# Kernel optimization log

Hardware: AMD Instinct MI355X
Metric: run time of the kernel (lower is better)

## Reference

```python
import jax, jax.numpy as jnp
import numpy as np

B, N, C = 128, 320, 768
H = 12
T = 64    # template tokens (8x8)
S = 256   # search tokens (16x16)


def setup_inputs() -> dict:
    key = jax.random.key(0)
    k1, k2, k3, k4 = jax.random.split(key, 4)
    return {
        "x1": jax.random.normal(k1, (B, N, C), dtype=jnp.float32),
        "x2": jax.random.normal(k2, (B, N, C), dtype=jnp.float32),
        "qkv_w": jax.random.normal(k3, (3 * C, C), dtype=jnp.float32) * 0.02,
        "proj_w": jax.random.normal(k4, (C, C), dtype=jnp.float32) * 0.02,
        "proj_b": jnp.zeros((C,), dtype=jnp.float32),
    }


def reference(x1, x2, qkv_w, proj_w, proj_b):
    # concat template tokens from x1 with search tokens from x2
    x = jnp.concatenate([x1[:, :T, :], x2[:, T:, :]], axis=1)  # [B, N, C]
    b, n, c = x.shape
    d = c // H
    scale = d ** -0.5

    qkv = (x @ qkv_w.T).reshape(b, n, 3, H, d).transpose(2, 0, 3, 1, 4)  # [3,B,H,N,D]
    q, k, v = qkv[0], qkv[1], qkv[2]

    # template -> template self-attention
    q_mt, k_mt, v_mt = q[:, :, :T], k[:, :, :T], v[:, :, :T]
    attn_mt = jax.nn.softmax(jnp.einsum('bhtd,bhsd->bhts', q_mt, k_mt) * scale, axis=-1)
    x_mt = jnp.einsum('bhts,bhsd->bhtd', attn_mt, v_mt).transpose(0, 2, 1, 3).reshape(b, T, c)

    # search -> all cross+self attention
    q_s = q[:, :, T:]
    attn_s = jax.nn.softmax(jnp.einsum('bhqd,bhkd->bhqk', q_s, k) * scale, axis=-1)
    x_s = jnp.einsum('bhqk,bhkd->bhqd', attn_s, v).transpose(0, 2, 1, 3).reshape(b, S, c)

    out = jnp.concatenate([x_mt, x_s], axis=1) @ proj_w.T + proj_b
    return out
```

## Files before the change

kernel.cpp:

```cpp
#include <hip/hip_runtime.h>
#include <hip/hip_bf16.h>
#include <stdint.h>

#define B_   128
#define N_   320
#define C_   768
#define H_   12
#define D_   64
#define NT_  (B_*N_)
#define K3_  (3*C_)
#define NKT  12
#define TE   (256*64)

typedef __attribute__((ext_vector_type(8))) __bf16 bf16x8;
typedef __attribute__((ext_vector_type(4))) float  f32x4;

__device__ __forceinline__ unsigned short f2bf(float f) {
  union { float f; unsigned u; } v; v.f = f;
  return (unsigned short)((v.u + 0x7fffu + ((v.u >> 16) & 1u)) >> 16);
}

__device__ __forceinline__ void gload16(const unsigned short* g, unsigned short* l) {
  __builtin_amdgcn_global_load_lds((const __attribute__((address_space(1))) void*)g,
                                   (__attribute__((address_space(3))) void*)l,
                                   16, 0, 0);
}

__global__ void prep_x(const float* __restrict__ x1, const float* __restrict__ x2,
                       unsigned short* __restrict__ xb) {
  const unsigned total4 = (unsigned)NT_ * C_ / 4;
  const unsigned stride = gridDim.x * blockDim.x;
  for (unsigned i = blockIdx.x * blockDim.x + threadIdx.x; i < total4; i += stride) {
    unsigned tok = i / (C_ / 4);
    unsigned n   = tok % N_;
    const float* src = (n < 64u) ? x1 : x2;
    float4 v = *(const float4*)(src + (size_t)i * 4u);
    ushort4 o;
    o.x = f2bf(v.x); o.y = f2bf(v.y); o.z = f2bf(v.z); o.w = f2bf(v.w);
    *(ushort4*)(xb + (size_t)i * 4u) = o;
  }
}

__global__ void prep_w(const float* __restrict__ qkv_w, const float* __restrict__ proj_w,
                       unsigned short* __restrict__ wq, unsigned short* __restrict__ wp) {
  const int QKV4 = (K3_ * C_) / 4;
  const int Q4   = (C_ * C_) / 4;
  const int P4   = (C_ * C_) / 4;
  int i = blockIdx.x * 256 + threadIdx.x;
  if (i < QKV4) {
    float s = (i < Q4) ? 0.125f : 1.0f;
    float4 v = *(const float4*)(qkv_w + (size_t)i * 4);
    ushort4 o;
    o.x = f2bf(v.x * s); o.y = f2bf(v.y * s); o.z = f2bf(v.z * s); o.w = f2bf(v.w * s);
    *(ushort4*)(wq + (size_t)i * 4) = o;
  } else if (i < QKV4 + P4) {
    int j = i - QKV4;
    float4 v = *(const float4*)(proj_w + (size_t)j * 4);
    ushort4 o;
    o.x = f2bf(v.x); o.y = f2bf(v.y); o.z = f2bf(v.z); o.w = f2bf(v.w);
    *(ushort4*)(wp + (size_t)j * 4) = o;
  }
}

#define BARR do { asm volatile("" ::: "memory"); __builtin_amdgcn_s_barrier(); asm volatile("" ::: "memory"); } while(0)
#define VMW(n) asm volatile("s_waitcnt vmcnt(" #n ")" ::: "memory")
#define PRIO1 __builtin_amdgcn_s_setprio(1)
#define PRIO0 __builtin_amdgcn_s_setprio(0)
#define RD(base, off) (*(const bf16x8*)((base) + (off)))

#define LDA_Q(ARR, QQ, PARX) do { \
    ARR[0][0] = RD(bAk0, (PARX)*32768 + (QQ)*8192);        \
    ARR[0][1] = RD(bAk1, (PARX)*32768 + (QQ)*8192);        \
    ARR[1][0] = RD(bAk0, (PARX)*32768 + (QQ)*8192 + 2048); \
    ARR[1][1] = RD(bAk1, (PARX)*32768 + (QQ)*8192 + 2048); } while(0)

#define LDB(PARX) do { \
    _Pragma("unroll") for (int nf = 0; nf < 4; ++nf) { \
      b_[0][nf] = RD(bBk0, (PARX)*32768 + nf*2048); \
      b_[1][nf] = RD(bBk1, (PARX)*32768 + nf*2048); } } while(0)

#define MFN(ARR, QQ) do { \
    _Pragma("unroll") for (int ks = 0; ks < 2; ++ks) \
    _Pragma("unroll") for (int f = 0; f < 2; ++f) \
    _Pragma("unroll") for (int nf = 0; nf < 4; ++nf) \
      acc[(QQ)*2+f][nf] = __builtin_amdgcn_mfma_f32_16x16x32_bf16(ARR[f][ks], b_[ks][nf], acc[(QQ)*2+f][nf], 0, 0, 0); \
  } while(0)

#define MFS(ARR, QQ) do { \
    _Pragma("unroll") for (int ks = 0; ks < 2; ++ks) \
    _Pragma("unroll") for (int f = 0; f < 2; ++f) \
    _Pragma("unroll") for (int nf = 0; nf < 4; ++nf) \
      acc[(QQ)*2+f][nf] = __builtin_amdgcn_mfma_f32_16x16x32_bf16(b_[ks][nf], ARR[f][ks], acc[(QQ)*2+f][nf], 0, 0, 0); \
  } while(0)

#define STGA4(PARX) do { \
    gload16(gA00, dA + ((PARX)^1)*TE);        gload16(gA01, dA + ((PARX)^1)*TE + 512);  \
    gload16(gA10, dA + ((PARX)^1)*TE + 8192); gload16(gA11, dA + ((PARX)^1)*TE + 8704); \
    gA00 += 64; gA01 += 64; gA10 += 64; gA11 += 64; } while(0)
#define STGB4(PARX) do { \
    gload16(gB00, dB + ((PARX)^1)*TE);        gload16(gB01, dB + ((PARX)^1)*TE + 512);  \
    gload16(gB10, dB + ((PARX)^1)*TE + 8192); gload16(gB11, dB + ((PARX)^1)*TE + 8704); \
    gB00 += 64; gB01 += 64; gB10 += 64; gB11 += 64; } while(0)
#define STG8(PARX) do { STGA4(PARX); STGB4(PARX); } while(0)

#define KT1(MF, PARX, STG_) do { \
    LDB(PARX); LDA_Q(aL_, 0, PARX); \
    STG_; \
    LDA_Q(aH_, 1, PARX); \
    PRIO1; MF(aL_, 0); PRIO0; \
    LDA_Q(aL_, 2, PARX); \
    PRIO1; MF(aH_, 1); PRIO0; \
    LDA_Q(aH_, 3, PARX); \
    PRIO1; MF(aL_, 2); PRIO0; \
    PRIO1; MF(aH_, 3); PRIO0; \
    VMW(0); BARR; \
  } while(0)

#define RESETA do { \
    gA00 = Ag_ + (size_t)row0n*768 + offA00; gA01 = Ag_ + (size_t)row0n*768 + offA01; \
    gA10 = Ag_ + (size_t)row0n*768 + offA10; gA11 = Ag_ + (size_t)row0n*768 + offA11; } while(0)
#define RESETB do { \
    gB00 = Wg_ + (size_t)col0n*768 + offA00; gB01 = Wg_ + (size_t)col0n*768 + offA01; \
    gB10 = Wg_ + (size_t)col0n*768 + offA10; gB11 = Wg_ + (size_t)col0n*768 + offA11; } while(0)

#define TILE12(MF) do { \
    _Pragma("unroll 1") for (int tt = 0; tt < 5; ++tt) { \
      KT1(MF, 0, STG8(0)); \
      KT1(MF, 1, STG8(1)); \
    } \
    KT1(MF, 0, STG8(0)); \
    KT1(MF, 1, { RESETA; RESETB; STG8(1); }); \
  } while(0)

#define GEMM_SETUP \
  const int tid = threadIdx.x, lane = tid & 63, w = tid >> 6; \
  const int wr = w >> 2, wc = w & 3; \
  const int lr = lane & 15, kg = lane >> 4; \
  const int rr = lane >> 3; \
  const int sp = (lane & 7) ^ rr; \
  const char* bAk0 = (const char*)As + wr*4096 + lr*128 + ((0*4 + kg) ^ (lr & 7))*16; \
  const char* bAk1 = (const char*)As + wr*4096 + lr*128 + ((1*4 + kg) ^ (lr & 7))*16; \
  const char* bBk0 = (const char*)Bs + wc*8192 + lr*128 + ((0*4 + kg) ^ (lr & 7))*16; \
  const char* bBk1 = (const char*)Bs + wc*8192 + lr*128 + ((1*4 + kg) ^ (lr & 7))*16; \
  const size_t offA00 = (size_t)(w*16 + rr)*768 + sp*8; \
  const size_t offA01 = offA00 + (size_t)8*768; \
  const size_t offA10 = offA00 + (size_t)128*768; \
  const size_t offA11 = offA01 + (size_t)128*768; \
  unsigned short* dA = As + w*1024; \
  unsigned short* dB = Bs + w*1024; \
  const unsigned short *gA00, *gA01, *gA10, *gA11, *gB00, *gB01, *gB10, *gB11;

#define GEMM_PROLOGUE(row0i, col0i) do { \
    gA00 = Ag_ + (size_t)(row0i)*768 + offA00; gA01 = Ag_ + (size_t)(row0i)*768 + offA01; \
    gA10 = Ag_ + (size_t)(row0i)*768 + offA10; gA11 = Ag_ + (size_t)(row0i)*768 + offA11; \
    gB00 = Wg_ + (size_t)(col0i)*768 + offA00; gB01 = Wg_ + (size_t)(col0i)*768 + offA01; \
    gB10 = Wg_ + (size_t)(col0i)*768 + offA10; gB11 = Wg_ + (size_t)(col0i)*768 + offA11; \
    STG8(1); \
    VMW(0); BARR; \
  } while(0)

#define ACC_ZERO do { \
    _Pragma("unroll") for (int mf = 0; mf < 8; ++mf) \
    _Pragma("unroll") for (int nf = 0; nf < 4; ++nf) acc[mf][nf] = vzero; } while(0)

__global__ void __launch_bounds__(512) gemm_qkv(const unsigned short* __restrict__ A,
                                                const unsigned short* __restrict__ W,
                                                unsigned short* __restrict__ qb,
                                                unsigned short* __restrict__ kb,
                                                unsigned short* __restrict__ vb) {
  __shared__ __align__(16) unsigned short As[2 * TE];
  __shared__ __align__(16) unsigned short Bs[2 * TE];
  GEMM_SETUP
  const unsigned short* Ag_ = A;
  const unsigned short* Wg_ = W;
  const int wv = blockIdx.x / 80;
  const int lb = blockIdx.x - wv * 80;

  const f32x4 vzero = {0.f, 0.f, 0.f, 0.f};
  f32x4 acc[8][4];
  ACC_ZERO;
  bf16x8 aL_[2][2], aH_[2][2], b_[2][4];

  {
    const int t0i = lb * 6;
    const int row0i = (t0i / 3) * 256, col0i = (wv * 3 + t0i % 3) * 256;
    GEMM_PROLOGUE(row0i, col0i);
  }

  if (wv != 2) {
    unsigned short* dst = (wv == 0) ? qb : kb;
#pragma unroll 1
    for (int j = 0; j < 6; ++j) {
      const int t = lb * 6 + j, tn = (j < 5) ? t + 1 : t;
      const int row0c = (t / 3) * 256, cb = (t % 3) * 256;
      const int row0n = (tn / 3) * 256, col0n = (wv * 3 + tn % 3) * 256;
      TILE12(MFS);
#pragma unroll
      for (int mf = 0; mf < 8; ++mf) {
        const int tok = row0c + (mf >> 1) * 64 + wr * 32 + (mf & 1) * 16 + lr;
        const unsigned bq = (unsigned)tok / 320u;
        const int tt2 = tok - (int)bq * 320;
#pragma unroll
        for (int nf = 0; nf < 4; ++nf) {
          const int nn = cb + wc * 64 + nf * 16 + kg * 4;
          const int h = nn >> 6, dd = nn & 63;
          ushort4 o;
          o.x = f2bf(acc[mf][nf][0]); o.y = f2bf(acc[mf][nf][1]);
          o.z = f2bf(acc[mf][nf][2]); o.w = f2bf(acc[mf][nf][3]);
          *(ushort4*)&dst[(size_t)((((int)bq * 12 + h) * 320 + tt2) * 64 + dd)] = o;
        }
      }
      ACC_ZERO;
    }
  } else {
#pragma unroll 1
    for (int j = 0; j < 6; ++j) {
      const int t = lb * 6 + j, tn = (j < 5) ? t + 1 : t;
      const int row0c = (t / 3) * 256, cb = (t % 3) * 256;
      const int row0n = (tn / 3) * 256, col0n = (wv * 3 + tn % 3) * 256;
      TILE12(MFN);
#pragma unroll
      for (int mf = 0; mf < 8; ++mf) {
        const int m0 = row0c + (mf >> 1) * 64 + wr * 32 + (mf & 1) * 16 + kg * 4;
        const unsigned bq = (unsigned)m0 / 320u;
        const int t0v = m0 - (int)bq * 320;
#pragma unroll
        for (int nf = 0; nf < 4; ++nf) {
          const int nn = cb + wc * 64 + nf * 16 + lr;
          const int h = nn >> 6, dd = nn & 63;
          ushort4 o;
          o.x = f2bf(acc[mf][nf][0]); o.y = f2bf(acc[mf][nf][1]);
          o.z = f2bf(acc[mf][nf][2]); o.w = f2bf(acc[mf][nf][3]);
          *(ushort4*)&vb[(size_t)(((((int)bq * 12 + h) * 64 + dd) * 320) + t0v)] = o;
        }
      }
      ACC_ZERO;
    }
  }
  asm volatile("s_waitcnt vmcnt(0) lgkmcnt(0)" ::: "memory");
}

__global__ void __launch_bounds__(256) attn(const unsigned short* __restrict__ qb,
                                            const unsigned short* __restrict__ kb,
                                            const unsigned short* __restrict__ vb,
                                            unsigned short* __restrict__ ab) {
  __shared__ __align__(16) unsigned short Ks[64 * 64];
  __shared__ __align__(16) unsigned short Vt[64 * 64];
  __shared__ __align__(16) unsigned short Pl[4 * 16 * 64];
  const int bid = blockIdx.x;
  const int qt = bid % 5, bh = bid / 5;
  const int tid = threadIdx.x, lane = tid & 63, w = tid >> 6;
  const int lr = lane & 15, kg = lane >> 4;

  const int qrow = qt * 64 + w * 16 + lr;
  const unsigned short* qptr = qb + (bh * 320 + qrow) * 64;
  const bf16x8 qa0 = *(const bf16x8*)(qptr + kg * 8);
  const bf16x8 qa1 = *(const bf16x8*)(qptr + 32 + kg * 8);

  f32x4 o[4] = {};
  float mrun[4] = {-1e30f, -1e30f, -1e30f, -1e30f};
  float lrun[4] = {0.f, 0.f, 0.f, 0.f};
  const int nchunk = (qt == 0) ? 1 : 5;

  const int c0 = w, c1 = w + 4;
  const int srow0 = c0 * 8 + (lane >> 3);
  const int srow1 = c1 * 8 + (lane >> 3);
  const int slot  = lane & 7;
  const int part0 = slot ^ (srow0 & 7);
  const int part1 = slot ^ (srow1 & 7);
  const unsigned short* kbase = kb + bh * 320 * 64;
  const unsigned short* vbase = vb + bh * 64 * 320;
  unsigned short* lk0 = &Ks[c0 * 512];
  unsigned short* lk1 = &Ks[c1 * 512];
  unsigned short* lv0 = &Vt[c0 * 512];
  unsigned short* lv1 = &Vt[c1 * 512];
  char* PwB = (char*)&Pl[w * 1024];

  for (int kc = 0; kc < nchunk; kc++) {
    gload16(kbase + (kc * 64 + srow0) * 64 + part0 * 8, lk0);
    gload16(kbase + (kc * 64 + srow1) * 64 + part1 * 8, lk1);
    gload16(vbase + srow0 * 320 + kc * 64 + part0 * 8, lv0);
    gload16(vbase + srow1 * 320 + kc * 64 + part1 * 8, lv1);
    __syncthreads();

    f32x4 s[4];
#pragma unroll
    for (int kt = 0; kt < 4; kt++) {
      const int key = kt * 16 + lr;
      const char* kr = (const char*)Ks + key * 128;
      const unsigned sw = (unsigned)((key & 7) << 4);
      bf16x8 k0 = *(const bf16x8*)(kr + ((kg * 16) ^ sw));
      bf16x8 k1 = *(const bf16x8*)(kr + ((64 + kg * 16) ^ sw));
      f32x4 z = {0.f, 0.f, 0.f, 0.f};
      z = __builtin_amdgcn_mfma_f32_16x16x32_bf16(qa0, k0, z, 0, 0, 0);
      z = __builtin_amdgcn_mfma_f32_16x16x32_bf16(qa1, k1, z, 0, 0, 0);
      s[kt] = z;
    }

#pragma unroll
    for (int r = 0; r < 4; r++) {
      float rm = fmaxf(fmaxf(s[0][r], s[1][r]), fmaxf(s[2][r], s[3][r]));
      rm = fmaxf(rm, __shfl_xor(rm, 1));
      rm = fmaxf(rm, __shfl_xor(rm, 2));
      rm = fmaxf(rm, __shfl_xor(rm, 4));
      rm = fmaxf(rm, __shfl_xor(rm, 8));
      const float mn = fmaxf(mrun[r], rm);
      const float alpha = __expf(mrun[r] - mn);
      mrun[r] = mn;
      const int q = kg * 4 + r;
      char* prow = PwB + q * 128;
      const unsigned sw = (unsigned)((q & 7) << 4);
      float rs = 0.f;
#pragma unroll
      for (int kt = 0; kt < 4; kt++) {
        const float p = __expf(s[kt][r] - mn);
        rs += p;
        const int key = kt * 16 + lr;
        *(unsigned short*)(prow + ((key * 2) ^ sw)) = f2bf(p);
      }
      rs += __shfl_xor(rs, 1);
      rs += __shfl_xor(rs, 2);
      rs += __shfl_xor(rs, 4);
      rs += __shfl_xor(rs, 8);
      lrun[r] = lrun[r] * alpha + rs;
#pragma unroll
      for (int dt = 0; dt < 4; dt++) o[dt][r] *= alpha;
    }

    asm volatile("s_waitcnt lgkmcnt(0)" ::: "memory");

    {
      const char* par = (const char*)PwB + lr * 128;
      const unsigned swp = (unsigned)((lr & 7) << 4);
      bf16x8 p0 = *(const bf16x8*)(par + ((kg * 16) ^ swp));
      bf16x8 p1 = *(const bf16x8*)(par + ((64 + kg * 16) ^ swp));
#pragma unroll
      for (int dt = 0; dt < 4; dt++) {
        const int d = dt * 16 + lr;
        const char* vr = (const char*)Vt + d * 128;
        const unsigned swv = (unsigned)((d & 7) << 4);
        bf16x8 v0 = *(const bf16x8*)(vr + ((kg * 16) ^ swv));
        bf16x8 v1 = *(const bf16x8*)(vr + ((64 + kg * 16) ^ swv));
        o[dt] = __builtin_amdgcn_mfma_f32_16x16x32_bf16(p0, v0, o[dt], 0, 0, 0);
        o[dt] = __builtin_amdgcn_mfma_f32_16x16x32_bf16(p1, v1, o[dt], 0, 0, 0);
      }
    }
    __syncthreads();
  }

  const int b = bh / 12, h = bh - b * 12;
#pragma unroll
  for (int r = 0; r < 4; r++) {
    const float inv = 1.0f / lrun[r];
    const int token = b * 320 + qt * 64 + w * 16 + kg * 4 + r;
    unsigned short* orow = ab + token * 768 + h * 64;
#pragma unroll
    for (int dt = 0; dt < 4; dt++)
      orow[dt * 16 + lr] = f2bf(o[dt][r] * inv);
  }
}

__global__ void __launch_bounds__(512) gemm_proj(const unsigned short* __restrict__ A,
                                                 const unsigned short* __restrict__ W,
                                                 const float* __restrict__ bias,
                                                 float* __restrict__ out) {
  __shared__ __align__(16) unsigned short As[2 * TE];
  __shared__ __align__(16) unsigned short Bs[2 * TE];
  GEMM_SETUP
  const unsigned short* Ag_ = A;
  const unsigned short* Wg_ = W;
  const int lb = blockIdx.x;

  const f32x4 vzero = {0.f, 0.f, 0.f, 0.f};
  f32x4 acc[8][4];
  ACC_ZERO;
  bf16x8 aL_[2][2], aH_[2][2], b_[2][4];

  {
    const int t0i = lb * 2;
    const int row0i = (t0i / 3) * 256, col0i = (t0i % 3) * 256;
    GEMM_PROLOGUE(row0i, col0i);
  }

#pragma unroll 1
  for (int j = 0; j < 2; ++j) {
    const int t = lb * 2 + j, tn = (j < 1) ? t + 1 : t;
    const int row0c = (t / 3) * 256, col0c = (t % 3) * 256;
    const int row0n = (tn / 3) * 256, col0n = (tn % 3) * 256;
    TILE12(MFN);
#pragma unroll
    for (int nf = 0; nf < 4; ++nf) {
      const int nn = col0c + wc * 64 + nf * 16 + lr;
      const float bv = bias[nn];
#pragma unroll
      for (int mf = 0; mf < 8; ++mf) {
        const int m0 = row0c + (mf >> 1) * 64 + wr * 32 + (mf & 1) * 16 + kg * 4;
        float* po = out + (size_t)m0 * 768 + nn;
#pragma unroll
        for (int r = 0; r < 4; r++)
          po[(size_t)r * 768] = acc[mf][nf][r] + bv;
      }
    }
    ACC_ZERO;
  }
  asm volatile("s_waitcnt vmcnt(0) lgkmcnt(0)" ::: "memory");
}

extern "C" void kernel_launch(void* const* d_in, const int* in_sizes, int n_in,
                              void* d_out, int out_size, void* d_ws, size_t ws_size,
                              hipStream_t stream) {
  (void)in_sizes; (void)n_in; (void)out_size; (void)ws_size;
  const float* x1     = (const float*)d_in[0];
  const float* x2     = (const float*)d_in[1];
  const float* qkv_w  = (const float*)d_in[2];
  const float* proj_w = (const float*)d_in[3];
  const float* proj_b = (const float*)d_in[4];
  float* out = (float*)d_out;

  const size_t TOK = (size_t)NT_ * C_;
  unsigned short* xb = (unsigned short*)d_ws;
  unsigned short* qb = xb + TOK;
  unsigned short* kb = qb + TOK;
  unsigned short* vb = kb + TOK;
  unsigned short* ab = vb + TOK;
  unsigned short* wq = ab + TOK;
  unsigned short* wp = wq + (size_t)K3_ * C_;

  prep_x<<<8192, 256, 0, stream>>>(x1, x2, xb);
  prep_w<<<2304, 256, 0, stream>>>(qkv_w, proj_w, wq, wp);
  gemm_qkv<<<240, 512, 0, stream>>>(xb, wq, qb, kb, vb);
  attn<<<1536 * 5, 256, 0, stream>>>(qb, kb, vb, ab);
  gemm_proj<<<240, 512, 0, stream>>>(ab, wp, proj_b, out);
}
```

Baseline: 406.7 us.

## Shrink GEMM tiles to 128x128 with 256 threads and fuse attention per (b,h)

Both GEMMs move from 256x256 tiles with 512-thread blocks to 128x128 tiles with 256-thread blocks, and 480 persistent blocks now each cover more tiles. The attention kernel goes from five blocks per (batch, head) to one 512-thread block per (batch, head), so each K/V chunk is loaded into shared memory once and reused by all query tiles. Warps split the 20 query tiles unevenly, and template tiles skip later key chunks. The aims are better occupancy and load balance in the GEMMs and less redundant K/V traffic in attention. The cost is less data reuse per GEMM tile and uneven per-warp work in attention.

```diff
diff --git a/kernel.cpp b/kernel.cpp
--- a/kernel.cpp
+++ b/kernel.cpp
@@ -9,8 +9,7 @@
 #define D_   64
 #define NT_  (B_*N_)
 #define K3_  (3*C_)
-#define NKT  12
-#define TE   (256*64)
+#define TE1  8192
 
 typedef __attribute__((ext_vector_type(8))) __bf16 bf16x8;
 typedef __attribute__((ext_vector_type(4))) float  f32x4;
@@ -63,150 +62,129 @@
 }
 
 #define BARR do { asm volatile("" ::: "memory"); __builtin_amdgcn_s_barrier(); asm volatile("" ::: "memory"); } while(0)
-#define VMW(n) asm volatile("s_waitcnt vmcnt(" #n ")" ::: "memory")
+#define VMW0 asm volatile("s_waitcnt vmcnt(0)" ::: "memory")
 #define PRIO1 __builtin_amdgcn_s_setprio(1)
 #define PRIO0 __builtin_amdgcn_s_setprio(0)
 #define RD(base, off) (*(const bf16x8*)((base) + (off)))
 
-#define LDA_Q(ARR, QQ, PARX) do { \
-    ARR[0][0] = RD(bAk0, (PARX)*32768 + (QQ)*8192);        \
-    ARR[0][1] = RD(bAk1, (PARX)*32768 + (QQ)*8192);        \
-    ARR[1][0] = RD(bAk0, (PARX)*32768 + (QQ)*8192 + 2048); \
-    ARR[1][1] = RD(bAk1, (PARX)*32768 + (QQ)*8192 + 2048); } while(0)
-
-#define LDB(PARX) do { \
-    _Pragma("unroll") for (int nf = 0; nf < 4; ++nf) { \
-      b_[0][nf] = RD(bBk0, (PARX)*32768 + nf*2048); \
-      b_[1][nf] = RD(bBk1, (PARX)*32768 + nf*2048); } } while(0)
-
-#define MFN(ARR, QQ) do { \
-    _Pragma("unroll") for (int ks = 0; ks < 2; ++ks) \
-    _Pragma("unroll") for (int f = 0; f < 2; ++f) \
-    _Pragma("unroll") for (int nf = 0; nf < 4; ++nf) \
-      acc[(QQ)*2+f][nf] = __builtin_amdgcn_mfma_f32_16x16x32_bf16(ARR[f][ks], b_[ks][nf], acc[(QQ)*2+f][nf], 0, 0, 0); \
+#define LD_A(PARX) do { _Pragma("unroll") for (int mi = 0; mi < 4; ++mi) { \
+    a_[mi][0] = RD(bAk0, (PARX)*16384 + mi*2048); \
+    a_[mi][1] = RD(bAk1, (PARX)*16384 + mi*2048); } } while(0)
+#define LD_B(PARX) do { _Pragma("unroll") for (int ni = 0; ni < 4; ++ni) { \
+    b_[0][ni] = RD(bBk0, (PARX)*16384 + ni*2048); \
+    b_[1][ni] = RD(bBk1, (PARX)*16384 + ni*2048); } } while(0)
+
+#define MFN1 do { _Pragma("unroll") for (int ks = 0; ks < 2; ++ks) \
+    _Pragma("unroll") for (int mi = 0; mi < 4; ++mi) \
+    _Pragma("unroll") for (int ni = 0; ni < 4; ++ni) \
+      acc[mi][ni] = __builtin_amdgcn_mfma_f32_16x16x32_bf16(a_[mi][ks], b_[ks][ni], acc[mi][ni], 0, 0, 0); } while(0)
+#define MFS1 do { _Pragma("unroll") for (int ks = 0; ks < 2; ++ks) \
+    _Pragma("unroll") for (int mi = 0; mi < 4; ++mi) \
+    _Pragma("unroll") for (int ni = 0; ni < 4; ++ni) \
+      acc[mi][ni] = __builtin_amdgcn_mfma_f32_16x16x32_bf16(b_[ks][ni], a_[mi][ks], acc[mi][ni], 0, 0, 0); } while(0)
+
+#define STG8_(BUFX) do { \
+    gload16(gA0, dA + (BUFX)*TE1);        gload16(gA1, dA + (BUFX)*TE1 + 512);  \
+    gload16(gA2, dA + (BUFX)*TE1 + 1024); gload16(gA3, dA + (BUFX)*TE1 + 1536); \
+    gload16(gB0, dB + (BUFX)*TE1);        gload16(gB1, dB + (BUFX)*TE1 + 512);  \
+    gload16(gB2, dB + (BUFX)*TE1 + 1024); gload16(gB3, dB + (BUFX)*TE1 + 1536); \
+    gA0 += 64; gA1 += 64; gA2 += 64; gA3 += 64; \
+    gB0 += 64; gB1 += 64; gB2 += 64; gB3 += 64; } while(0)
+
+#define KT128(MF, PARX, STG_) do { \
+    STG_; \
+    LD_B(PARX); LD_A(PARX); \
+    PRIO1; MF; PRIO0; \
+    VMW0; BARR; \
   } while(0)
 
-#define MFS(ARR, QQ) do { \
-    _Pragma("unroll") for (int ks = 0; ks < 2; ++ks) \
-    _Pragma("unroll") for (int f = 0; f < 2; ++f) \
-    _Pragma("unroll") for (int nf = 0; nf < 4; ++nf) \
-      acc[(QQ)*2+f][nf] = __builtin_amdgcn_mfma_f32_16x16x32_bf16(b_[ks][nf], ARR[f][ks], acc[(QQ)*2+f][nf], 0, 0, 0); \
-  } while(0)
-
-#define STGA4(PARX) do { \
-    gload16(gA00, dA + ((PARX)^1)*TE);        gload16(gA01, dA + ((PARX)^1)*TE + 512);  \
-    gload16(gA10, dA + ((PARX)^1)*TE + 8192); gload16(gA11, dA + ((PARX)^1)*TE + 8704); \
-    gA00 += 64; gA01 += 64; gA10 += 64; gA11 += 64; } while(0)
-#define STGB4(PARX) do { \
-    gload16(gB00, dB + ((PARX)^1)*TE);        gload16(gB01, dB + ((PARX)^1)*TE + 512);  \
-    gload16(gB10, dB + ((PARX)^1)*TE + 8192); gload16(gB11, dB + ((PARX)^1)*TE + 8704); \
-    gB00 += 64; gB01 += 64; gB10 += 64; gB11 += 64; } while(0)
-#define STG8(PARX) do { STGA4(PARX); STGB4(PARX); } while(0)
-
-#define KT1(MF, PARX, STG_) do { \
-    LDB(PARX); LDA_Q(aL_, 0, PARX); \
-    STG_; \
-    LDA_Q(aH_, 1, PARX); \
-    PRIO1; MF(aL_, 0); PRIO0; \
-    LDA_Q(aL_, 2, PARX); \
-    PRIO1; MF(aH_, 1); PRIO0; \
-    LDA_Q(aH_, 3, PARX); \
-    PRIO1; MF(aL_, 2); PRIO0; \
-    PRIO1; MF(aH_, 3); PRIO0; \
-    VMW(0); BARR; \
-  } while(0)
-
-#define RESETA do { \
-    gA00 = Ag_ + (size_t)row0n*768 + offA00; gA01 = Ag_ + (size_t)row0n*768 + offA01; \
-    gA10 = Ag_ + (size_t)row0n*768 + offA10; gA11 = Ag_ + (size_t)row0n*768 + offA11; } while(0)
-#define RESETB do { \
-    gB00 = Wg_ + (size_t)col0n*768 + offA00; gB01 = Wg_ + (size_t)col0n*768 + offA01; \
-    gB10 = Wg_ + (size_t)col0n*768 + offA10; gB11 = Wg_ + (size_t)col0n*768 + offA11; } while(0)
+#define RESETN do { \
+    gA0 = Ag_ + (size_t)row0n*768 + offG0; gA1 = Ag_ + (size_t)row0n*768 + offG1; \
+    gA2 = Ag_ + (size_t)row0n*768 + offG2; gA3 = Ag_ + (size_t)row0n*768 + offG3; \
+    gB0 = Wg_ + (size_t)col0n*768 + offG0; gB1 = Wg_ + (size_t)col0n*768 + offG1; \
+    gB2 = Wg_ + (size_t)col0n*768 + offG2; gB3 = Wg_ + (size_t)col0n*768 + offG3; } while(0)
 
 #define TILE12(MF) do { \
     _Pragma("unroll 1") for (int tt = 0; tt < 5; ++tt) { \
-      KT1(MF, 0, STG8(0)); \
-      KT1(MF, 1, STG8(1)); \
+      KT128(MF, 0, STG8_(1)); \
+      KT128(MF, 1, STG8_(0)); \
     } \
-    KT1(MF, 0, STG8(0)); \
-    KT1(MF, 1, { RESETA; RESETB; STG8(1); }); \
+    KT128(MF, 0, STG8_(1)); \
+    KT128(MF, 1, { RESETN; STG8_(0); }); \
   } while(0)
 
 #define GEMM_SETUP \
   const int tid = threadIdx.x, lane = tid & 63, w = tid >> 6; \
-  const int wr = w >> 2, wc = w & 3; \
+  const int wr = w >> 1, wc = w & 1; \
   const int lr = lane & 15, kg = lane >> 4; \
   const int rr = lane >> 3; \
   const int sp = (lane & 7) ^ rr; \
-  const char* bAk0 = (const char*)As + wr*4096 + lr*128 + ((0*4 + kg) ^ (lr & 7))*16; \
-  const char* bAk1 = (const char*)As + wr*4096 + lr*128 + ((1*4 + kg) ^ (lr & 7))*16; \
+  const char* bAk0 = (const char*)As + wr*8192 + lr*128 + ((0*4 + kg) ^ (lr & 7))*16; \
+  const char* bAk1 = (const char*)As + wr*8192 + lr*128 + ((1*4 + kg) ^ (lr & 7))*16; \
   const char* bBk0 = (const char*)Bs + wc*8192 + lr*128 + ((0*4 + kg) ^ (lr & 7))*16; \
   const char* bBk1 = (const char*)Bs + wc*8192 + lr*128 + ((1*4 + kg) ^ (lr & 7))*16; \
-  const size_t offA00 = (size_t)(w*16 + rr)*768 + sp*8; \
-  const size_t offA01 = offA00 + (size_t)8*768; \
-  const size_t offA10 = offA00 + (size_t)128*768; \
-  const size_t offA11 = offA01 + (size_t)128*768; \
-  unsigned short* dA = As + w*1024; \
-  unsigned short* dB = Bs + w*1024; \
-  const unsigned short *gA00, *gA01, *gA10, *gA11, *gB00, *gB01, *gB10, *gB11;
+  const size_t offG0 = (size_t)(w*32 +  0 + rr)*768 + sp*8; \
+  const size_t offG1 = (size_t)(w*32 +  8 + rr)*768 + sp*8; \
+  const size_t offG2 = (size_t)(w*32 + 16 + rr)*768 + sp*8; \
+  const size_t offG3 = (size_t)(w*32 + 24 + rr)*768 + sp*8; \
+  unsigned short* dA = As + w*2048; \
+  unsigned short* dB = Bs + w*2048; \
+  const unsigned short *gA0, *gA1, *gA2, *gA3, *gB0, *gB1, *gB2, *gB3;
 
 #define GEMM_PROLOGUE(row0i, col0i) do { \
-    gA00 = Ag_ + (size_t)(row0i)*768 + offA00; gA01 = Ag_ + (size_t)(row0i)*768 + offA01; \
-    gA10 = Ag_ + (size_t)(row0i)*768 + offA10; gA11 = Ag_ + (size_t)(row0i)*768 + offA11; \
-    gB00 = Wg_ + (size_t)(col0i)*768 + offA00; gB01 = Wg_ + (size_t)(col0i)*768 + offA01; \
-    gB10 = Wg_ + (size_t)(col0i)*768 + offA10; gB11 = Wg_ + (size_t)(col0i)*768 + offA11; \
-    STG8(1); \
-    VMW(0); BARR; \
+    gA0 = Ag_ + (size_t)(row0i)*768 + offG0; gA1 = Ag_ + (size_t)(row0i)*768 + offG1; \
+    gA2 = Ag_ + (size_t)(row0i)*768 + offG2; gA3 = Ag_ + (size_t)(row0i)*768 + offG3; \
+    gB0 = Wg_ + (size_t)(col0i)*768 + offG0; gB1 = Wg_ + (size_t)(col0i)*768 + offG1; \
+    gB2 = Wg_ + (size_t)(col0i)*768 + offG2; gB3 = Wg_ + (size_t)(col0i)*768 + offG3; \
+    STG8_(0); \
+    VMW0; BARR; \
   } while(0)
 
 #define ACC_ZERO do { \
-    _Pragma("unroll") for (int mf = 0; mf < 8; ++mf) \
-    _Pragma("unroll") for (int nf = 0; nf < 4; ++nf) acc[mf][nf] = vzero; } while(0)
-
-__global__ void __launch_bounds__(512) gemm_qkv(const unsigned short* __restrict__ A,
+    _Pragma("unroll") for (int mi = 0; mi < 4; ++mi) \
+    _Pragma("unroll") for (int ni = 0; ni < 4; ++ni) acc[mi][ni] = vzero; } while(0)
+
+__global__ void __launch_bounds__(256) gemm_qkv(const unsigned short* __restrict__ A,
                                                 const unsigned short* __restrict__ W,
                                                 unsigned short* __restrict__ qb,
                                                 unsigned short* __restrict__ kb,
                                                 unsigned short* __restrict__ vb) {
-  __shared__ __align__(16) unsigned short As[2 * TE];
-  __shared__ __align__(16) unsigned short Bs[2 * TE];
+  __shared__ __align__(16) unsigned short As[2 * TE1];
+  __shared__ __align__(16) unsigned short Bs[2 * TE1];
   GEMM_SETUP
   const unsigned short* Ag_ = A;
   const unsigned short* Wg_ = W;
-  const int wv = blockIdx.x / 80;
-  const int lb = blockIdx.x - wv * 80;
+  const int r  = blockIdx.x / 160;
+  const int pp = blockIdx.x - r * 160;
+  const int bm0 = pp * 2;
 
   const f32x4 vzero = {0.f, 0.f, 0.f, 0.f};
-  f32x4 acc[8][4];
+  f32x4 acc[4][4];
   ACC_ZERO;
-  bf16x8 aL_[2][2], aH_[2][2], b_[2][4];
-
-  {
-    const int t0i = lb * 6;
-    const int row0i = (t0i / 3) * 256, col0i = (wv * 3 + t0i % 3) * 256;
-    GEMM_PROLOGUE(row0i, col0i);
-  }
-
-  if (wv != 2) {
-    unsigned short* dst = (wv == 0) ? qb : kb;
+  bf16x8 a_[4][2], b_[2][4];
+
+  GEMM_PROLOGUE(bm0 * 128, r * 768 + 0 * 128);
+
+  if (r != 2) {
+    unsigned short* dst = (r == 0) ? qb : kb;
 #pragma unroll 1
-    for (int j = 0; j < 6; ++j) {
-      const int t = lb * 6 + j, tn = (j < 5) ? t + 1 : t;
-      const int row0c = (t / 3) * 256, cb = (t % 3) * 256;
-      const int row0n = (tn / 3) * 256, col0n = (wv * 3 + tn % 3) * 256;
-      TILE12(MFS);
-#pragma unroll
-      for (int mf = 0; mf < 8; ++mf) {
-        const int tok = row0c + (mf >> 1) * 64 + wr * 32 + (mf & 1) * 16 + lr;
+    for (int j = 0; j < 12; ++j) {
+      const int jn = (j < 11) ? j + 1 : j;
+      const int row0  = (bm0 + (j  / 6)) * 128, cb  = (j  % 6) * 128;
+      const int row0n = (bm0 + (jn / 6)) * 128, col0n = r * 768 + (jn % 6) * 128;
+      TILE12(MFS1);
+#pragma unroll
+      for (int mi = 0; mi < 4; ++mi) {
+        const int tok = row0 + wr * 64 + mi * 16 + lr;
         const unsigned bq = (unsigned)tok / 320u;
         const int tt2 = tok - (int)bq * 320;
 #pragma unroll
-        for (int nf = 0; nf < 4; ++nf) {
-          const int nn = cb + wc * 64 + nf * 16 + kg * 4;
+        for (int ni = 0; ni < 4; ++ni) {
+          const int nn = cb + wc * 64 + ni * 16 + kg * 4;
           const int h = nn >> 6, dd = nn & 63;
           ushort4 o;
-          o.x = f2bf(acc[mf][nf][0]); o.y = f2bf(acc[mf][nf][1]);
-          o.z = f2bf(acc[mf][nf][2]); o.w = f2bf(acc[mf][nf][3]);
+          o.x = f2bf(acc[mi][ni][0]); o.y = f2bf(acc[mi][ni][1]);
+          o.z = f2bf(acc[mi][ni][2]); o.w = f2bf(acc[mi][ni][3]);
           *(ushort4*)&dst[(size_t)((((int)bq * 12 + h) * 320 + tt2) * 64 + dd)] = o;
         }
       }
@@ -214,23 +192,23 @@
     }
   } else {
 #pragma unroll 1
-    for (int j = 0; j < 6; ++j) {
-      const int t = lb * 6 + j, tn = (j < 5) ? t + 1 : t;
-      const int row0c = (t / 3) * 256, cb = (t % 3) * 256;
-      const int row0n = (tn / 3) * 256, col0n = (wv * 3 + tn % 3) * 256;
-      TILE12(MFN);
-#pragma unroll
-      for (int mf = 0; mf < 8; ++mf) {
-        const int m0 = row0c + (mf >> 1) * 64 + wr * 32 + (mf & 1) * 16 + kg * 4;
+    for (int j = 0; j < 12; ++j) {
+      const int jn = (j < 11) ? j + 1 : j;
+      const int row0  = (bm0 + (j  / 6)) * 128, cb  = (j  % 6) * 128;
+      const int row0n = (bm0 + (jn / 6)) * 128, col0n = r * 768 + (jn % 6) * 128;
+      TILE12(MFN1);
+#pragma unroll
+      for (int mi = 0; mi < 4; ++mi) {
+        const int m0 = row0 + wr * 64 + mi * 16 + kg * 4;
         const unsigned bq = (unsigned)m0 / 320u;
         const int t0v = m0 - (int)bq * 320;
 #pragma unroll
-        for (int nf = 0; nf < 4; ++nf) {
-          const int nn = cb + wc * 64 + nf * 16 + lr;
+        for (int ni = 0; ni < 4; ++ni) {
+          const int nn = cb + wc * 64 + ni * 16 + lr;
           const int h = nn >> 6, dd = nn & 63;
           ushort4 o;
-          o.x = f2bf(acc[mf][nf][0]); o.y = f2bf(acc[mf][nf][1]);
-          o.z = f2bf(acc[mf][nf][2]); o.w = f2bf(acc[mf][nf][3]);
+          o.x = f2bf(acc[mi][ni][0]); o.y = f2bf(acc[mi][ni][1]);
+          o.z = f2bf(acc[mi][ni][2]); o.w = f2bf(acc[mi][ni][3]);
           *(ushort4*)&vb[(size_t)(((((int)bq * 12 + h) * 64 + dd) * 320) + t0v)] = o;
         }
       }
@@ -240,109 +218,115 @@
   asm volatile("s_waitcnt vmcnt(0) lgkmcnt(0)" ::: "memory");
 }
 
-__global__ void __launch_bounds__(256) attn(const unsigned short* __restrict__ qb,
+__global__ void __launch_bounds__(512) attn(const unsigned short* __restrict__ qb,
                                             const unsigned short* __restrict__ kb,
                                             const unsigned short* __restrict__ vb,
                                             unsigned short* __restrict__ ab) {
   __shared__ __align__(16) unsigned short Ks[64 * 64];
   __shared__ __align__(16) unsigned short Vt[64 * 64];
-  __shared__ __align__(16) unsigned short Pl[4 * 16 * 64];
-  const int bid = blockIdx.x;
-  const int qt = bid % 5, bh = bid / 5;
+  __shared__ __align__(16) unsigned short Pl[8 * 16 * 64];
+  const int bh = blockIdx.x;
   const int tid = threadIdx.x, lane = tid & 63, w = tid >> 6;
   const int lr = lane & 15, kg = lane >> 4;
-
-  const int qrow = qt * 64 + w * 16 + lr;
-  const unsigned short* qptr = qb + (bh * 320 + qrow) * 64;
-  const bf16x8 qa0 = *(const bf16x8*)(qptr + kg * 8);
-  const bf16x8 qa1 = *(const bf16x8*)(qptr + 32 + kg * 8);
-
-  f32x4 o[4] = {};
-  float mrun[4] = {-1e30f, -1e30f, -1e30f, -1e30f};
-  float lrun[4] = {0.f, 0.f, 0.f, 0.f};
-  const int nchunk = (qt == 0) ? 1 : 5;
-
-  const int c0 = w, c1 = w + 4;
-  const int srow0 = c0 * 8 + (lane >> 3);
-  const int srow1 = c1 * 8 + (lane >> 3);
-  const int slot  = lane & 7;
-  const int part0 = slot ^ (srow0 & 7);
-  const int part1 = slot ^ (srow1 & 7);
-  const unsigned short* kbase = kb + bh * 320 * 64;
-  const unsigned short* vbase = vb + bh * 64 * 320;
-  unsigned short* lk0 = &Ks[c0 * 512];
-  unsigned short* lk1 = &Ks[c1 * 512];
-  unsigned short* lv0 = &Vt[c0 * 512];
-  unsigned short* lv1 = &Vt[c1 * 512];
+  const int nt = (w < 4) ? 3 : 2;
+  const int tix0 = w, tix1 = w + 8, tix2 = (w < 4) ? (w + 16) : w;
+
+  const unsigned short* qB = qb + (size_t)bh * 320 * 64;
+  bf16x8 qa0[3], qa1[3];
+  {
+    const unsigned short* p0 = qB + (tix0 * 16 + lr) * 64;
+    qa0[0] = *(const bf16x8*)(p0 + kg * 8); qa1[0] = *(const bf16x8*)(p0 + 32 + kg * 8);
+    const unsigned short* p1 = qB + (tix1 * 16 + lr) * 64;
+    qa0[1] = *(const bf16x8*)(p1 + kg * 8); qa1[1] = *(const bf16x8*)(p1 + 32 + kg * 8);
+    const unsigned short* p2 = qB + (tix2 * 16 + lr) * 64;
+    qa0[2] = *(const bf16x8*)(p2 + kg * 8); qa1[2] = *(const bf16x8*)(p2 + 32 + kg * 8);
+  }
+
+  f32x4 o[3][4] = {};
+  float rm_[3][4], rl_[3][4];
+#pragma unroll
+  for (int s = 0; s < 3; ++s)
+#pragma unroll
+    for (int rq = 0; rq < 4; ++rq) { rm_[s][rq] = -1e30f; rl_[s][rq] = 0.f; }
+
+  const int rr = lane >> 3;
+  const int part = (lane & 7) ^ rr;
+  const int srow = w * 8 + rr;
+  const unsigned short* kbase = kb + (size_t)bh * 320 * 64;
+  const unsigned short* vbase = vb + (size_t)bh * 64 * 320;
+  unsigned short* lk = &Ks[w * 512];
+  unsigned short* lv = &Vt[w * 512];
   char* PwB = (char*)&Pl[w * 1024];
 
-  for (int kc = 0; kc < nchunk; kc++) {
-    gload16(kbase + (kc * 64 + srow0) * 64 + part0 * 8, lk0);
-    gload16(kbase + (kc * 64 + srow1) * 64 + part1 * 8, lk1);
-    gload16(vbase + srow0 * 320 + kc * 64 + part0 * 8, lv0);
-    gload16(vbase + srow1 * 320 + kc * 64 + part1 * 8, lv1);
+#pragma unroll 1
+  for (int kc = 0; kc < 5; kc++) {
+    gload16(kbase + (kc * 64 + srow) * 64 + part * 8, lk);
+    gload16(vbase + srow * 320 + kc * 64 + part * 8, lv);
     __syncthreads();
 
-    f32x4 s[4];
-#pragma unroll
-    for (int kt = 0; kt < 4; kt++) {
-      const int key = kt * 16 + lr;
-      const char* kr = (const char*)Ks + key * 128;
-      const unsigned sw = (unsigned)((key & 7) << 4);
-      bf16x8 k0 = *(const bf16x8*)(kr + ((kg * 16) ^ sw));
-      bf16x8 k1 = *(const bf16x8*)(kr + ((64 + kg * 16) ^ sw));
-      f32x4 z = {0.f, 0.f, 0.f, 0.f};
-      z = __builtin_amdgcn_mfma_f32_16x16x32_bf16(qa0, k0, z, 0, 0, 0);
-      z = __builtin_amdgcn_mfma_f32_16x16x32_bf16(qa1, k1, z, 0, 0, 0);
-      s[kt] = z;
-    }
-
-#pragma unroll
-    for (int r = 0; r < 4; r++) {
-      float rm = fmaxf(fmaxf(s[0][r], s[1][r]), fmaxf(s[2][r], s[3][r]));
-      rm = fmaxf(rm, __shfl_xor(rm, 1));
-      rm = fmaxf(rm, __shfl_xor(rm, 2));
-      rm = fmaxf(rm, __shfl_xor(rm, 4));
-      rm = fmaxf(rm, __shfl_xor(rm, 8));
-      const float mn = fmaxf(mrun[r], rm);
-      const float alpha = __expf(mrun[r] - mn);
-      mrun[r] = mn;
-      const int q = kg * 4 + r;
-      char* prow = PwB + q * 128;
-      const unsigned sw = (unsigned)((q & 7) << 4);
-      float rs = 0.f;
-#pragma unroll
-      for (int kt = 0; kt < 4; kt++) {
-        const float p = __expf(s[kt][r] - mn);
-        rs += p;
-        const int key = kt * 16 + lr;
-        *(unsigned short*)(prow + ((key * 2) ^ sw)) = f2bf(p);
-      }
-      rs += __shfl_xor(rs, 1);
-      rs += __shfl_xor(rs, 2);
-      rs += __shfl_xor(rs, 4);
-      rs += __shfl_xor(rs, 8);
-      lrun[r] = lrun[r] * alpha + rs;
-#pragma unroll
-      for (int dt = 0; dt < 4; dt++) o[dt][r] *= alpha;
-    }
-
-    asm volatile("s_waitcnt lgkmcnt(0)" ::: "memory");
-
-    {
-      const char* par = (const char*)PwB + lr * 128;
-      const unsigned swp = (unsigned)((lr & 7) << 4);
-      bf16x8 p0 = *(const bf16x8*)(par + ((kg * 16) ^ swp));
-      bf16x8 p1 = *(const bf16x8*)(par + ((64 + kg * 16) ^ swp));
-#pragma unroll
-      for (int dt = 0; dt < 4; dt++) {
-        const int d = dt * 16 + lr;
-        const char* vr = (const char*)Vt + d * 128;
-        const unsigned swv = (unsigned)((d & 7) << 4);
-        bf16x8 v0 = *(const bf16x8*)(vr + ((kg * 16) ^ swv));
-        bf16x8 v1 = *(const bf16x8*)(vr + ((64 + kg * 16) ^ swv));
-        o[dt] = __builtin_amdgcn_mfma_f32_16x16x32_bf16(p0, v0, o[dt], 0, 0, 0);
-        o[dt] = __builtin_amdgcn_mfma_f32_16x16x32_bf16(p1, v1, o[dt], 0, 0, 0);
+#pragma unroll
+    for (int s = 0; s < 3; ++s) {
+      const bool active = (s < nt) && !(s == 0 && w < 4 && kc > 0);
+      if (active) {
+        f32x4 sv[4];
+#pragma unroll
+        for (int kt = 0; kt < 4; kt++) {
+          const int key = kt * 16 + lr;
+          const char* kr = (const char*)Ks + key * 128;
+          const unsigned sw = (unsigned)((key & 7) << 4);
+          bf16x8 k0 = *(const bf16x8*)(kr + ((kg * 16) ^ sw));
+          bf16x8 k1 = *(const bf16x8*)(kr + ((64 + kg * 16) ^ sw));
+          f32x4 z = {0.f, 0.f, 0.f, 0.f};
+          z = __builtin_amdgcn_mfma_f32_16x16x32_bf16(qa0[s], k0, z, 0, 0, 0);
+          z = __builtin_amdgcn_mfma_f32_16x16x32_bf16(qa1[s], k1, z, 0, 0, 0);
+          sv[kt] = z;
+        }
+#pragma unroll
+        for (int rq = 0; rq < 4; rq++) {
+          float rm = fmaxf(fmaxf(sv[0][rq], sv[1][rq]), fmaxf(sv[2][rq], sv[3][rq]));
+          rm = fmaxf(rm, __shfl_xor(rm, 1));
+          rm = fmaxf(rm, __shfl_xor(rm, 2));
+          rm = fmaxf(rm, __shfl_xor(rm, 4));
+          rm = fmaxf(rm, __shfl_xor(rm, 8));
+          const float mn = fmaxf(rm_[s][rq], rm);
+          const float alpha = __expf(rm_[s][rq] - mn);
+          rm_[s][rq] = mn;
+          const int q = kg * 4 + rq;
+          char* prow = PwB + q * 128;
+          const unsigned sw = (unsigned)((q & 7) << 4);
+          float rs = 0.f;
+#pragma unroll
+          for (int kt = 0; kt < 4; kt++) {
+            const float p = __expf(sv[kt][rq] - mn);
+            rs += p;
+            const int key = kt * 16 + lr;
+            *(unsigned short*)(prow + ((key * 2) ^ sw)) = f2bf(p);
+          }
+          rs += __shfl_xor(rs, 1);
+          rs += __shfl_xor(rs, 2);
+          rs += __shfl_xor(rs, 4);
+          rs += __shfl_xor(rs, 8);
+          rl_[s][rq] = rl_[s][rq] * alpha + rs;
+#pragma unroll
+          for (int dt = 0; dt < 4; dt++) o[s][dt][rq] *= alpha;
+        }
+        asm volatile("s_waitcnt lgkmcnt(0)" ::: "memory");
+        {
+          const char* par = (const char*)PwB + lr * 128;
+          const unsigned swp = (unsigned)((lr & 7) << 4);
+          bf16x8 p0 = *(const bf16x8*)(par + ((kg * 16) ^ swp));
+          bf16x8 p1 = *(const bf16x8*)(par + ((64 + kg * 16) ^ swp));
+#pragma unroll
+          for (int dt = 0; dt < 4; dt++) {
+            const int d = dt * 16 + lr;
+            const char* vr = (const char*)Vt + d * 128;
+            const unsigned swv = (unsigned)((d & 7) << 4);
+            bf16x8 v0 = *(const bf16x8*)(vr + ((kg * 16) ^ swv));
+            bf16x8 v1 = *(const bf16x8*)(vr + ((64 + kg * 16) ^ swv));
+            o[s][dt] = __builtin_amdgcn_mfma_f32_16x16x32_bf16(p0, v0, o[s][dt], 0, 0, 0);
+            o[s][dt] = __builtin_amdgcn_mfma_f32_16x16x32_bf16(p1, v1, o[s][dt], 0, 0, 0);
+          }
+        }
       }
     }
     __syncthreads();
@@ -350,55 +334,58 @@
 
   const int b = bh / 12, h = bh - b * 12;
 #pragma unroll
-  for (int r = 0; r < 4; r++) {
-    const float inv = 1.0f / lrun[r];
-    const int token = b * 320 + qt * 64 + w * 16 + kg * 4 + r;
-    unsigned short* orow = ab + token * 768 + h * 64;
-#pragma unroll
-    for (int dt = 0; dt < 4; dt++)
-      orow[dt * 16 + lr] = f2bf(o[dt][r] * inv);
-  }
-}
-
-__global__ void __launch_bounds__(512) gemm_proj(const unsigned short* __restrict__ A,
+  for (int s = 0; s < 3; ++s) {
+    if (s < nt) {
+      const int tix = (s == 0) ? tix0 : (s == 1) ? tix1 : tix2;
+#pragma unroll
+      for (int rq = 0; rq < 4; rq++) {
+        const float inv = 1.0f / rl_[s][rq];
+        const int token = b * 320 + tix * 16 + kg * 4 + rq;
+        unsigned short* orow = ab + (size_t)token * 768 + h * 64;
+#pragma unroll
+        for (int dt = 0; dt < 4; dt++)
+          orow[dt * 16 + lr] = f2bf(o[s][dt][rq] * inv);
+      }
+    }
+  }
+}
+
+__global__ void __launch_bounds__(256) gemm_proj(const unsigned short* __restrict__ A,
                                                  const unsigned short* __restrict__ W,
                                                  const float* __restrict__ bias,
                                                  float* __restrict__ out) {
-  __shared__ __align__(16) unsigned short As[2 * TE];
-  __shared__ __align__(16) unsigned short Bs[2 * TE];
+  __shared__ __align__(16) unsigned short As[2 * TE1];
+  __shared__ __align__(16) unsigned short Bs[2 * TE1];
   GEMM_SETUP
   const unsigned short* Ag_ = A;
   const unsigned short* Wg_ = W;
-  const int lb = blockIdx.x;
+  const int bnp = blockIdx.x % 3;
+  const int bm0 = (blockIdx.x / 3) * 2;
 
   const f32x4 vzero = {0.f, 0.f, 0.f, 0.f};
-  f32x4 acc[8][4];
+  f32x4 acc[4][4];
   ACC_ZERO;
-  bf16x8 aL_[2][2], aH_[2][2], b_[2][4];
-
-  {
-    const int t0i = lb * 2;
-    const int row0i = (t0i / 3) * 256, col0i = (t0i % 3) * 256;
-    GEMM_PROLOGUE(row0i, col0i);
-  }
+  bf16x8 a_[4][2], b_[2][4];
+
+  GEMM_PROLOGUE(bm0 * 128, (bnp * 2) * 128);
 
 #pragma unroll 1
-  for (int j = 0; j < 2; ++j) {
-    const int t = lb * 2 + j, tn = (j < 1) ? t + 1 : t;
-    const int row0c = (t / 3) * 256, col0c = (t % 3) * 256;
-    const int row0n = (tn / 3) * 256, col0n = (tn % 3) * 256;
-    TILE12(MFN);
-#pragma unroll
-    for (int nf = 0; nf < 4; ++nf) {
-      const int nn = col0c + wc * 64 + nf * 16 + lr;
+  for (int j = 0; j < 4; ++j) {
+    const int jn = (j < 3) ? j + 1 : j;
+    const int row0  = (bm0 + (j  >> 1)) * 128, col0  = (bnp * 2 + (j  & 1)) * 128;
+    const int row0n = (bm0 + (jn >> 1)) * 128, col0n = (bnp * 2 + (jn & 1)) * 128;
+    TILE12(MFN1);
+#pragma unroll
+    for (int ni = 0; ni < 4; ++ni) {
+      const int nn = col0 + wc * 64 + ni * 16 + lr;
       const float bv = bias[nn];
 #pragma unroll
-      for (int mf = 0; mf < 8; ++mf) {
-        const int m0 = row0c + (mf >> 1) * 64 + wr * 32 + (mf & 1) * 16 + kg * 4;
+      for (int mi = 0; mi < 4; ++mi) {
+        const int m0 = row0 + wr * 64 + mi * 16 + kg * 4;
         float* po = out + (size_t)m0 * 768 + nn;
 #pragma unroll
-        for (int r = 0; r < 4; r++)
-          po[(size_t)r * 768] = acc[mf][nf][r] + bv;
+        for (int rg = 0; rg < 4; rg++)
+          po[(size_t)rg * 768] = acc[mi][ni][rg] + bv;
       }
     }
     ACC_ZERO;
@@ -428,7 +415,7 @@
 
   prep_x<<<8192, 256, 0, stream>>>(x1, x2, xb);
   prep_w<<<2304, 256, 0, stream>>>(qkv_w, proj_w, wq, wp);
-  gemm_qkv<<<240, 512, 0, stream>>>(xb, wq, qb, kb, vb);
-  attn<<<1536 * 5, 256, 0, stream>>>(qb, kb, vb, ab);
-  gemm_proj<<<240, 512, 0, stream>>>(ab, wp, proj_b, out);
-}
+  gemm_qkv<<<480, 256, 0, stream>>>(xb, wq, qb, kb, vb);
+  attn<<<1536, 512, 0, stream>>>(qb, kb, vb, ab);
+  gemm_proj<<<480, 256, 0, stream>>>(ab, wp, proj_b, out);
+}
```

Result: slower. 675.7 us (+66.2%).
